# Kernel tuning notes

Measured on AMD Instinct MI355X. Metric: run time of the kernel, lower is better.

The kernel has to match this reference:

```python
import jax, jax.numpy as jnp
import numpy as np

D_MODEL = 1024
NUM_HEADS = 16
HEAD_DIM = D_MODEL // NUM_HEADS


def setup_inputs() -> dict:
    key = jax.random.key(0)
    ks = jax.random.split(key, 9)
    s = 1.0 / np.sqrt(D_MODEL)
    x = jax.random.normal(ks[0], (2, 2048, D_MODEL), dtype=jnp.float32)
    Wq = jax.random.uniform(ks[1], (D_MODEL, D_MODEL), jnp.float32, -s, s)
    bq = jax.random.uniform(ks[2], (D_MODEL,), jnp.float32, -s, s)
    Wk = jax.random.uniform(ks[3], (D_MODEL, D_MODEL), jnp.float32, -s, s)
    bk = jax.random.uniform(ks[4], (D_MODEL,), jnp.float32, -s, s)
    Wv = jax.random.uniform(ks[5], (D_MODEL, D_MODEL), jnp.float32, -s, s)
    bv = jax.random.uniform(ks[6], (D_MODEL,), jnp.float32, -s, s)
    Wo = jax.random.uniform(ks[7], (D_MODEL, D_MODEL), jnp.float32, -s, s)
    bo = jax.random.uniform(ks[8], (D_MODEL,), jnp.float32, -s, s)
    return {"x": x, "Wq": Wq, "bq": bq, "Wk": Wk, "bk": bk,
            "Wv": Wv, "bv": bv, "Wo": Wo, "bo": bo}


def reference(x, Wq, bq, Wk, bk, Wv, bv, Wo, bo):
    B, S, _ = x.shape
    def split_heads(t):  # [B,S,D] -> [B,H,S,hd]
        return t.reshape(B, S, NUM_HEADS, HEAD_DIM).transpose(0, 2, 1, 3)
    q = split_heads(x @ Wq + bq)
    k = split_heads(x @ Wk + bk)
    v = split_heads(x @ Wv + bv)
    scores = jnp.einsum('bhqd,bhkd->bhqk', q, k) / np.sqrt(HEAD_DIM)
    attn = jax.nn.softmax(scores, axis=-1)
    ctx = jnp.einsum('bhqk,bhkd->bhqd', attn, v)
    ctx = ctx.transpose(0, 2, 1, 3).reshape(B, S, D_MODEL)
    return ctx @ Wo + bo
```

## Files before the change

### kernel.cpp

```cpp
#include <hip/hip_runtime.h>
#include <stdint.h>

#define DM 1024
#define SEQ 2048
#define NTOK 4096
#define HD 64

typedef __bf16 bf16x8 __attribute__((ext_vector_type(8)));
typedef float f32x4 __attribute__((ext_vector_type(4)));
typedef uint32_t u32x2 __attribute__((ext_vector_type(2)));
typedef uint32_t u32x4 __attribute__((ext_vector_type(4)));

#if __has_builtin(__builtin_amdgcn_exp2f)
#define EXP2F(x) __builtin_amdgcn_exp2f(x)
#else
#define EXP2F(x) exp2f(x)
#endif

__device__ __forceinline__ void gll16f(const char* g, char* lds_wave_base, int lane) {
#if __has_builtin(__builtin_amdgcn_global_load_lds)
  __builtin_amdgcn_global_load_lds(
      (const __attribute__((address_space(1))) void*)g,
      (__attribute__((address_space(3))) void*)lds_wave_base, 16, 0, 0);
#else
  *(bf16x8*)(lds_wave_base + lane * 16) = *(const bf16x8*)g;
#endif
}

__device__ __forceinline__ uint16_t f2bf(float f) {
  uint32_t x = __float_as_uint(f);
  return (uint16_t)((x + 0x7fffu + ((x >> 16) & 1u)) >> 16);
}

__device__ __forceinline__ uint32_t cvtpk(float a, float b) {
  uint32_t r;
  asm("v_cvt_pk_bf16_f32 %0, %1, %2" : "=v"(r) : "v"(a), "v"(b));
  return r;
}

__device__ __forceinline__ bf16x8 mk8(uint32_t a, uint32_t b, uint32_t c, uint32_t d) {
  u32x4 t = {a, b, c, d};
  return __builtin_bit_cast(bf16x8, t);
}

__global__ void cvt_x_kernel(const float* __restrict__ x, uint16_t* __restrict__ xb) {
  int i = (blockIdx.x * 256 + threadIdx.x) * 4;
  float4 v = *(const float4*)&x[i];
  uint64_t pk = (uint64_t)f2bf(v.x) | ((uint64_t)f2bf(v.y) << 16) |
                ((uint64_t)f2bf(v.z) << 32) | ((uint64_t)f2bf(v.w) << 48);
  *(uint64_t*)&xb[i] = pk;
}

__global__ void twt4_kernel(const float* __restrict__ W0, const float* __restrict__ W1,
                            const float* __restrict__ W2, const float* __restrict__ W3,
                            uint16_t* __restrict__ T0, uint16_t* __restrict__ T1,
                            uint16_t* __restrict__ T2, uint16_t* __restrict__ T3) {
  __shared__ float t[32][33];
  int z = blockIdx.z;
  const float* W = (z == 0) ? W0 : (z == 1) ? W1 : (z == 2) ? W2 : W3;
  uint16_t* T = (z == 0) ? T0 : (z == 1) ? T1 : (z == 2) ? T2 : T3;
  int tx = threadIdx.x, ty = threadIdx.y;
  int kb = blockIdx.y * 32, nb = blockIdx.x * 32;
#pragma unroll
  for (int i = 0; i < 4; i++)
    t[ty + i * 8][tx] = W[(kb + ty + i * 8) * DM + nb + tx];
  __syncthreads();
#pragma unroll
  for (int i = 0; i < 4; i++)
    T[(nb + ty + i * 8) * DM + kb + tx] = f2bf(t[tx][ty + i * 8]);
}

template <int MODE, int MF>
__device__ __forceinline__ void gemm_body(const uint16_t* __restrict__ A,
                                          const uint16_t* __restrict__ Bt,
                                          const float* __restrict__ bias, float scale,
                                          void* __restrict__ out, uint16_t* lds) {
  const int tid = threadIdx.x;
  const int w = tid >> 6, lane = tid & 63;
  const int wr = w >> 1, wc = w & 1;
  const int a15 = lane & 15, a4 = lane >> 4;
  const int m0 = blockIdx.y * (MF * 32), n0 = blockIdx.x * 128;
  char* lgA = (char*)lds;
  char* lgB = (char*)(lds + MF * 2048);
  f32x4 acc[MF][4];
#pragma unroll
  for (int m = 0; m < MF; m++)
#pragma unroll
    for (int n = 0; n < 4; n++) acc[m][n] = (f32x4){0.f, 0.f, 0.f, 0.f};

  const char* Ag = (const char*)(A + (size_t)m0 * DM);
  const char* Bg = (const char*)(Bt + (size_t)n0 * DM);
  const int srow = lane >> 3;
  const int scol = ((lane & 7) * 16) ^ (srow << 4);
  const int swz = (a15 & 7) << 4;

  for (int k0 = 0; k0 < DM; k0 += 64) {
#pragma unroll
    for (int c = 0; c < MF; c++) {
      int ro = w * (MF * 8) + c * 8 + srow;
      gll16f(Ag + (size_t)ro * (DM * 2) + k0 * 2 + scol, lgA + (w * MF + c) * 1024, lane);
    }
#pragma unroll
    for (int c = 0; c < 4; c++) {
      int ro = w * 32 + c * 8 + srow;
      gll16f(Bg + (size_t)ro * (DM * 2) + k0 * 2 + scol, lgB + (w * 4 + c) * 1024, lane);
    }
    __syncthreads();
    bf16x8 af[MF][2], bfr[4][2];
#pragma unroll
    for (int m = 0; m < MF; m++)
#pragma unroll
      for (int kk = 0; kk < 2; kk++)
        af[m][kk] = *(const bf16x8*)(lgA + (wr * (MF * 16) + m * 16 + a15) * 128 +
                                     ((kk * 64 + a4 * 16) ^ swz));
#pragma unroll
    for (int n = 0; n < 4; n++)
#pragma unroll
      for (int kk = 0; kk < 2; kk++)
        bfr[n][kk] = *(const bf16x8*)(lgB + (wc * 64 + n * 16 + a15) * 128 +
                                      ((kk * 64 + a4 * 16) ^ swz));
#pragma unroll
    for (int kk = 0; kk < 2; kk++)
#pragma unroll
      for (int m = 0; m < MF; m++)
#pragma unroll
        for (int n = 0; n < 4; n++)
          acc[m][n] = __builtin_amdgcn_mfma_f32_16x16x32_bf16(af[m][kk], bfr[n][kk],
                                                              acc[m][n], 0, 0, 0);
    __syncthreads();
  }

#pragma unroll
  for (int m = 0; m < MF; m++) {
#pragma unroll
    for (int n = 0; n < 4; n++) {
      int gr0 = m0 + wr * (MF * 16) + m * 16 + a4 * 4;
      int col = n0 + wc * 64 + n * 16 + a15;
      float bv = bias[col];
      if constexpr (MODE == 2) {
        float* O = (float*)out;
#pragma unroll
        for (int j = 0; j < 4; j++)
          O[(size_t)(gr0 + j) * DM + col] = acc[m][n][j] + bv;
      } else if constexpr (MODE == 0) {
        uint16_t* O = (uint16_t*)out;
        int h = col >> 6, d = col & 63;
#pragma unroll
        for (int j = 0; j < 4; j++) {
          int gr = gr0 + j;
          int b = gr >> 11, s = gr & 2047;
          O[((size_t)(((b << 4) + h)) * SEQ + s) * HD + d] = f2bf((acc[m][n][j] + bv) * scale);
        }
      } else {
        uint16_t* O = (uint16_t*)out;
        int h = col >> 6, d = col & 63;
        int b = gr0 >> 11, s0 = gr0 & 2047;
        int it = s0 >> 6, s6 = s0 & 63;
        int pos = (s6 >> 5) * 32 + ((s6 >> 2) & 3) * 8 + ((s6 >> 4) & 1) * 4;
        uint64_t pk = 0;
#pragma unroll
        for (int j = 0; j < 4; j++)
          pk |= (uint64_t)f2bf(acc[m][n][j] + bv) << (16 * j);
        *(uint64_t*)&O[((size_t)(((b << 4) + h)) * HD + d) * SEQ + it * 64 + pos] = pk;
      }
    }
  }
}

#define CS_SCALE 0.180336880f

__global__ __launch_bounds__(256, 2) void gemm_qkv_kernel(
    const uint16_t* __restrict__ xb, const uint16_t* __restrict__ wtq,
    const uint16_t* __restrict__ wtk, const uint16_t* __restrict__ wtv,
    const float* __restrict__ bq, const float* __restrict__ bk,
    const float* __restrict__ bv, uint16_t* __restrict__ qo,
    uint16_t* __restrict__ ko, uint16_t* __restrict__ vto) {
  __shared__ __attribute__((aligned(16))) uint16_t lds[16384];
  int z = blockIdx.z;
  if (z == 0)      gemm_body<0, 4>(xb, wtq, bq, CS_SCALE, qo, lds);
  else if (z == 1) gemm_body<0, 4>(xb, wtk, bk, 1.0f, ko, lds);
  else             gemm_body<1, 4>(xb, wtv, bv, 1.0f, vto, lds);
}

__global__ __launch_bounds__(256, 2) void gemm_out_kernel(
    const uint16_t* __restrict__ ctx, const uint16_t* __restrict__ wto,
    const float* __restrict__ bo, float* __restrict__ out) {
  __shared__ __attribute__((aligned(16))) uint16_t lds[12288];
  gemm_body<2, 2>(ctx, wto, bo, 1.0f, out, lds);
}

__global__ __launch_bounds__(256, 2) void attn_kernel(
    const uint16_t* __restrict__ qg, const uint16_t* __restrict__ kg,
    const uint16_t* __restrict__ vtg, uint16_t* __restrict__ ctx) {
  const int tid = threadIdx.x;
  const int w = tid >> 6, l = tid & 63;
  const int l15 = l & 15, g = l >> 4;
  int id = blockIdx.x;
  int wg = (id & 7) * 64 + (id >> 3);
  int bh = wg >> 4, qb = wg & 15;
  const int q0 = qb * 128 + w * 32;
  const uint16_t* Qb = qg + (size_t)bh * SEQ * HD;
  const char* Kc = (const char*)(kg + (size_t)bh * SEQ * HD);
  const char* Vc = (const char*)(vtg + (size_t)bh * HD * SEQ);

  __shared__ __attribute__((aligned(16))) char Klds[2][8192];
  __shared__ __attribute__((aligned(16))) char Vlds[2][8192];

  const int srow = l >> 3;
  const int scolx = ((l & 7) * 16) ^ (srow << 4);

#define STAGE(BI, IT)                                                          \
  {                                                                            \
    const int it1_ = (IT);                                                     \
    _Pragma("unroll") for (int i = 0; i < 2; i++) {                            \
      int r = w * 16 + i * 8 + srow;                                           \
      gll16f(Kc + (size_t)(it1_ * 64 + r) * 128 + scolx,                       \
             &Klds[BI][w * 2048 + i * 1024], l);                               \
      gll16f(Vc + (size_t)r * (SEQ * 2) + it1_ * 128 + scolx,                  \
             &Vlds[BI][w * 2048 + i * 1024], l);                               \
    }                                                                          \
  }

  bf16x8 bq[2][2];
#pragma unroll
  for (int qs = 0; qs < 2; qs++)
#pragma unroll
    for (int ks = 0; ks < 2; ks++)
      bq[qs][ks] = *(const bf16x8*)&Qb[(size_t)(q0 + qs * 16 + l15) * HD + ks * 32 + g * 8];

  f32x4 o[4][2];
#pragma unroll
  for (int dt = 0; dt < 4; dt++)
#pragma unroll
    for (int qs = 0; qs < 2; qs++) o[dt][qs] = (f32x4){0.f, 0.f, 0.f, 0.f};
  f32x4 ol0 = {0.f, 0.f, 0.f, 0.f}, ol1 = {0.f, 0.f, 0.f, 0.f};
  const int swz = (l15 & 7) << 4;
  const uint32_t ONE2 = 0x3F803F80u;
  const bf16x8 aones = mk8(ONE2, ONE2, ONE2, ONE2);

  STAGE(0, 0);

#define ATTN_TILE(IT, BI, BN)                                                  \
  {                                                                            \
    const int it_ = (IT);                                                      \
    if (it_ + 1 < SEQ / 64) {                                                  \
      STAGE(BN, it_ + 1);                                                      \
      asm volatile("s_waitcnt vmcnt(4)\n\ts_barrier" ::: "memory");            \
    } else {                                                                   \
      asm volatile("s_waitcnt vmcnt(0)\n\ts_barrier" ::: "memory");            \
    }                                                                          \
                                            \
    bf16x8 ak[4][2];                                                           \
    _Pragma("unroll") for (int kt = 0; kt < 4; kt++)                           \
        _Pragma("unroll") for (int ks = 0; ks < 2; ks++)                       \
            ak[kt][ks] = *(const bf16x8*)&Klds[BI][(kt * 16 + l15) * 128 +     \
                                                   ((ks * 64 + g * 16) ^ swz)];\
                     \
    bf16x8 av[4][2];                                                           \
    _Pragma("unroll") for (int dt = 0; dt < 4; dt++)                           \
        _Pragma("unroll") for (int kb = 0; kb < 2; kb++)                       \
            av[dt][kb] = *(const bf16x8*)&Vlds[BI][(dt * 16 + l15) * 128 +     \
                                                   ((kb * 64 + g * 16) ^ swz)];\
                                           \
    f32x4 s[2][4];                                                             \
    _Pragma("unroll") for (int qs = 0; qs < 2; qs++)                           \
        _Pragma("unroll") for (int kt = 0; kt < 4; kt++)                       \
            s[qs][kt] = (f32x4){0.f, 0.f, 0.f, 0.f};                           \
    __builtin_amdgcn_s_setprio(1);                                             \
    _Pragma("unroll") for (int kt = 0; kt < 4; kt++)                           \
        _Pragma("unroll") for (int ks = 0; ks < 2; ks++) {                     \
      s[0][kt] = __builtin_amdgcn_mfma_f32_16x16x32_bf16(ak[kt][ks], bq[0][ks], s[0][kt], 0, 0, 0); \
      s[1][kt] = __builtin_amdgcn_mfma_f32_16x16x32_bf16(ak[kt][ks], bq[1][ks], s[1][kt], 0, 0, 0); \
    }                                                                          \
    __builtin_amdgcn_s_setprio(0);                                             \
        \
    float p0[4][4], p1[4][4];                                                  \
    _Pragma("unroll") for (int kt = 0; kt < 4; kt++)                           \
        _Pragma("unroll") for (int j = 0; j < 4; j++) {                        \
      p0[kt][j] = EXP2F(s[0][kt][j]);                                          \
      p1[kt][j] = EXP2F(s[1][kt][j]);                                          \
    }                                                                          \
    bf16x8 bp0[2], bp1[2];                                                     \
    _Pragma("unroll") for (int kb = 0; kb < 2; kb++) {                         \
      bp0[kb] = mk8(cvtpk(p0[2 * kb][0], p0[2 * kb][1]),                       \
                    cvtpk(p0[2 * kb][2], p0[2 * kb][3]),                       \
                    cvtpk(p0[2 * kb + 1][0], p0[2 * kb + 1][1]),               \
                    cvtpk(p0[2 * kb + 1][2], p0[2 * kb + 1][3]));              \
      bp1[kb] = mk8(cvtpk(p1[2 * kb][0], p1[2 * kb][1]),                       \
                    cvtpk(p1[2 * kb][2], p1[2 * kb][3]),                       \
                    cvtpk(p1[2 * kb + 1][0], p1[2 * kb + 1][1]),               \
                    cvtpk(p1[2 * kb + 1][2], p1[2 * kb + 1][3]));              \
    }                                                                          \
                                                \
    __builtin_amdgcn_s_setprio(1);                                             \
    _Pragma("unroll") for (int dt = 0; dt < 4; dt++)                           \
        _Pragma("unroll") for (int kb = 0; kb < 2; kb++) {                     \
      o[dt][0] = __builtin_amdgcn_mfma_f32_16x16x32_bf16(av[dt][kb], bp0[kb], o[dt][0], 0, 0, 0); \
      o[dt][1] = __builtin_amdgcn_mfma_f32_16x16x32_bf16(av[dt][kb], bp1[kb], o[dt][1], 0, 0, 0); \
    }                                                                          \
    _Pragma("unroll") for (int kb = 0; kb < 2; kb++) {                         \
      ol0 = __builtin_amdgcn_mfma_f32_16x16x32_bf16(aones, bp0[kb], ol0, 0, 0, 0); \
      ol1 = __builtin_amdgcn_mfma_f32_16x16x32_bf16(aones, bp1[kb], ol1, 0, 0, 0); \
    }                                                                          \
    __builtin_amdgcn_s_setprio(0);                                             \
    asm volatile("s_waitcnt lgkmcnt(0)\n\ts_barrier" ::: "memory");            \
  }

  for (int it2 = 0; it2 < SEQ / 128; ++it2) {
    ATTN_TILE(2 * it2, 0, 1);
    ATTN_TILE(2 * it2 + 1, 1, 0);
  }
#undef ATTN_TILE
#undef STAGE

  float inv0 = 1.0f / ol0[0];
  float inv1 = 1.0f / ol1[0];
  int b = bh >> 4, h = bh & 15;
  uint16_t* cr0 = ctx + (size_t)(b * SEQ + q0 + l15) * DM + h * HD + 4 * g;
  uint16_t* cr1 = cr0 + (size_t)16 * DM;
#pragma unroll
  for (int dt = 0; dt < 4; dt++) {
    u32x2 wv;
    wv[0] = cvtpk(o[dt][0][0] * inv0, o[dt][0][1] * inv0);
    wv[1] = cvtpk(o[dt][0][2] * inv0, o[dt][0][3] * inv0);
    *(u32x2*)&cr0[dt * 16] = wv;
    u32x2 wv2;
    wv2[0] = cvtpk(o[dt][1][0] * inv1, o[dt][1][1] * inv1);
    wv2[1] = cvtpk(o[dt][1][2] * inv1, o[dt][1][3] * inv1);
    *(u32x2*)&cr1[dt * 16] = wv2;
  }
}

extern "C" void kernel_launch(void* const* d_in, const int* in_sizes, int n_in,
                              void* d_out, int out_size, void* d_ws, size_t ws_size,
                              hipStream_t stream) {
  const float* x  = (const float*)d_in[0];
  const float* Wq = (const float*)d_in[1];
  const float* bq = (const float*)d_in[2];
  const float* Wk = (const float*)d_in[3];
  const float* bk = (const float*)d_in[4];
  const float* Wv = (const float*)d_in[5];
  const float* bv = (const float*)d_in[6];
  const float* Wo = (const float*)d_in[7];
  const float* bo = (const float*)d_in[8];

  char* ws = (char*)d_ws;
  uint16_t* xb  = (uint16_t*)(ws);
  uint16_t* wtq = (uint16_t*)(ws + 8388608);
  uint16_t* wtk = (uint16_t*)(ws + 10485760);
  uint16_t* wtv = (uint16_t*)(ws + 12582912);
  uint16_t* wto = (uint16_t*)(ws + 14680064);
  uint16_t* qb  = (uint16_t*)(ws + 16777216);
  uint16_t* kb  = (uint16_t*)(ws + 25165824);
  uint16_t* vtb = (uint16_t*)(ws + 33554432);
  uint16_t* ctx = xb;

  cvt_x_kernel<<<dim3(4096), dim3(256), 0, stream>>>(x, xb);
  twt4_kernel<<<dim3(32, 32, 4), dim3(32, 8), 0, stream>>>(
      Wq, Wk, Wv, Wo, wtq, wtk, wtv, wto);
  gemm_qkv_kernel<<<dim3(8, 32, 3), dim3(256), 0, stream>>>(
      xb, wtq, wtk, wtv, bq, bk, bv, qb, kb, vtb);
  attn_kernel<<<dim3(512), dim3(256), 0, stream>>>(qb, kb, vtb, ctx);
  gemm_out_kernel<<<dim3(8, 64), dim3(256), 0, stream>>>(ctx, wto, bo, (float*)d_out);
}
```

Measured before the change: 96.08 us.

## Merge prep kernels, swizzle GEMM block order, and deepen attention K/V prefetch

```diff
diff --git a/kernel.cpp b/kernel.cpp
--- a/kernel.cpp
+++ b/kernel.cpp
@@ -43,24 +43,27 @@
   return __builtin_bit_cast(bf16x8, t);
 }
 
-__global__ void cvt_x_kernel(const float* __restrict__ x, uint16_t* __restrict__ xb) {
-  int i = (blockIdx.x * 256 + threadIdx.x) * 4;
-  float4 v = *(const float4*)&x[i];
-  uint64_t pk = (uint64_t)f2bf(v.x) | ((uint64_t)f2bf(v.y) << 16) |
-                ((uint64_t)f2bf(v.z) << 32) | ((uint64_t)f2bf(v.w) << 48);
-  *(uint64_t*)&xb[i] = pk;
-}
-
-__global__ void twt4_kernel(const float* __restrict__ W0, const float* __restrict__ W1,
+__global__ void prep_kernel(const float* __restrict__ x, uint16_t* __restrict__ xb,
+                            const float* __restrict__ W0, const float* __restrict__ W1,
                             const float* __restrict__ W2, const float* __restrict__ W3,
                             uint16_t* __restrict__ T0, uint16_t* __restrict__ T1,
                             uint16_t* __restrict__ T2, uint16_t* __restrict__ T3) {
   __shared__ float t[32][33];
-  int z = blockIdx.z;
-  const float* W = (z == 0) ? W0 : (z == 1) ? W1 : (z == 2) ? W2 : W3;
-  uint16_t* T = (z == 0) ? T0 : (z == 1) ? T1 : (z == 2) ? T2 : T3;
-  int tx = threadIdx.x, ty = threadIdx.y;
-  int kb = blockIdx.y * 32, nb = blockIdx.x * 32;
+  int bid = blockIdx.x;
+  if (bid < 4096) {
+    int i = (bid * 256 + threadIdx.x) * 4;
+    float4 v = *(const float4*)&x[i];
+    uint64_t pk = (uint64_t)f2bf(v.x) | ((uint64_t)f2bf(v.y) << 16) |
+                  ((uint64_t)f2bf(v.z) << 32) | ((uint64_t)f2bf(v.w) << 48);
+    *(uint64_t*)&xb[i] = pk;
+    return;
+  }
+  int b2 = bid - 4096;
+  int zz = b2 >> 10, rr = b2 & 1023;
+  const float* W = (zz == 0) ? W0 : (zz == 1) ? W1 : (zz == 2) ? W2 : W3;
+  uint16_t* T = (zz == 0) ? T0 : (zz == 1) ? T1 : (zz == 2) ? T2 : T3;
+  int tx = threadIdx.x & 31, ty = threadIdx.x >> 5;
+  int nb = (rr & 31) * 32, kb = (rr >> 5) * 32;
 #pragma unroll
   for (int i = 0; i < 4; i++)
     t[ty + i * 8][tx] = W[(kb + ty + i * 8) * DM + nb + tx];
@@ -74,12 +77,13 @@
 __device__ __forceinline__ void gemm_body(const uint16_t* __restrict__ A,
                                           const uint16_t* __restrict__ Bt,
                                           const float* __restrict__ bias, float scale,
-                                          void* __restrict__ out, uint16_t* lds) {
+                                          void* __restrict__ out, uint16_t* lds,
+                                          int bx, int by) {
   const int tid = threadIdx.x;
   const int w = tid >> 6, lane = tid & 63;
   const int wr = w >> 1, wc = w & 1;
   const int a15 = lane & 15, a4 = lane >> 4;
-  const int m0 = blockIdx.y * (MF * 32), n0 = blockIdx.x * 128;
+  const int m0 = by * (MF * 32), n0 = bx * 128;
   char* lgA = (char*)lds;
   char* lgB = (char*)(lds + MF * 2048);
   f32x4 acc[MF][4];
@@ -176,17 +180,23 @@
     const float* __restrict__ bv, uint16_t* __restrict__ qo,
     uint16_t* __restrict__ ko, uint16_t* __restrict__ vto) {
   __shared__ __attribute__((aligned(16))) uint16_t lds[16384];
-  int z = blockIdx.z;
-  if (z == 0)      gemm_body<0, 4>(xb, wtq, bq, CS_SCALE, qo, lds);
-  else if (z == 1) gemm_body<0, 4>(xb, wtk, bk, 1.0f, ko, lds);
-  else             gemm_body<1, 4>(xb, wtv, bv, 1.0f, vto, lds);
+  int id = blockIdx.x;
+  int swz = (id & 7) * 96 + (id >> 3);
+  int z = swz >> 8, r = swz & 255;
+  int by = r >> 3, bx = r & 7;
+  if (z == 0)      gemm_body<0, 4>(xb, wtq, bq, CS_SCALE, qo, lds, bx, by);
+  else if (z == 1) gemm_body<0, 4>(xb, wtk, bk, 1.0f, ko, lds, bx, by);
+  else             gemm_body<1, 4>(xb, wtv, bv, 1.0f, vto, lds, bx, by);
 }
 
 __global__ __launch_bounds__(256, 2) void gemm_out_kernel(
     const uint16_t* __restrict__ ctx, const uint16_t* __restrict__ wto,
     const float* __restrict__ bo, float* __restrict__ out) {
   __shared__ __attribute__((aligned(16))) uint16_t lds[12288];
-  gemm_body<2, 2>(ctx, wto, bo, 1.0f, out, lds);
+  int id = blockIdx.x;
+  int swz = (id & 7) * 64 + (id >> 3);
+  int by = swz >> 3, bx = swz & 7;
+  gemm_body<2, 2>(ctx, wto, bo, 1.0f, out, lds, bx, by);
 }
 
 __global__ __launch_bounds__(256, 2) void attn_kernel(
@@ -203,8 +213,8 @@
   const char* Kc = (const char*)(kg + (size_t)bh * SEQ * HD);
   const char* Vc = (const char*)(vtg + (size_t)bh * HD * SEQ);
 
-  __shared__ __attribute__((aligned(16))) char Klds[2][8192];
-  __shared__ __attribute__((aligned(16))) char Vlds[2][8192];
+  __shared__ __attribute__((aligned(16))) char Klds[4][8192];
+  __shared__ __attribute__((aligned(16))) char Vlds[4][8192];
 
   const int srow = l >> 3;
   const int scolx = ((l & 7) * 16) ^ (srow << 4);
@@ -238,17 +248,8 @@
   const uint32_t ONE2 = 0x3F803F80u;
   const bf16x8 aones = mk8(ONE2, ONE2, ONE2, ONE2);
 
-  STAGE(0, 0);
-
-#define ATTN_TILE(IT, BI, BN)                                                  \
+#define TILE_BODY(BI)                                                          \
   {                                                                            \
-    const int it_ = (IT);                                                      \
-    if (it_ + 1 < SEQ / 64) {                                                  \
-      STAGE(BN, it_ + 1);                                                      \
-      asm volatile("s_waitcnt vmcnt(4)\n\ts_barrier" ::: "memory");            \
-    } else {                                                                   \
-      asm volatile("s_waitcnt vmcnt(0)\n\ts_barrier" ::: "memory");            \
-    }                                                                          \
                                             \
     bf16x8 ak[4][2];                                                           \
     _Pragma("unroll") for (int kt = 0; kt < 4; kt++)                           \
@@ -303,14 +304,31 @@
       ol1 = __builtin_amdgcn_mfma_f32_16x16x32_bf16(aones, bp1[kb], ol1, 0, 0, 0); \
     }                                                                          \
     __builtin_amdgcn_s_setprio(0);                                             \
-    asm volatile("s_waitcnt lgkmcnt(0)\n\ts_barrier" ::: "memory");            \
-  }
-
-  for (int it2 = 0; it2 < SEQ / 128; ++it2) {
-    ATTN_TILE(2 * it2, 0, 1);
-    ATTN_TILE(2 * it2 + 1, 1, 0);
-  }
-#undef ATTN_TILE
+  }
+
+  STAGE(0, 0);
+  STAGE(1, 1);
+
+  for (int it4 = 0; it4 < 8; ++it4) {
+    int tb = it4 * 4;
+    STAGE(2, tb + 2);
+    STAGE(3, tb + 3);
+    asm volatile("s_waitcnt vmcnt(8)\n\ts_barrier" ::: "memory");
+    TILE_BODY(0);
+    TILE_BODY(1);
+    asm volatile("s_waitcnt lgkmcnt(0)\n\ts_barrier" ::: "memory");
+    if (it4 < 7) {
+      STAGE(0, tb + 4);
+      STAGE(1, tb + 5);
+      asm volatile("s_waitcnt vmcnt(8)\n\ts_barrier" ::: "memory");
+    } else {
+      asm volatile("s_waitcnt vmcnt(0)\n\ts_barrier" ::: "memory");
+    }
+    TILE_BODY(2);
+    TILE_BODY(3);
+    asm volatile("s_waitcnt lgkmcnt(0)\n\ts_barrier" ::: "memory");
+  }
+#undef TILE_BODY
 #undef STAGE
 
   float inv0 = 1.0f / ol0[0];
@@ -355,11 +373,10 @@
   uint16_t* vtb = (uint16_t*)(ws + 33554432);
   uint16_t* ctx = xb;
 
-  cvt_x_kernel<<<dim3(4096), dim3(256), 0, stream>>>(x, xb);
-  twt4_kernel<<<dim3(32, 32, 4), dim3(32, 8), 0, stream>>>(
-      Wq, Wk, Wv, Wo, wtq, wtk, wtv, wto);
-  gemm_qkv_kernel<<<dim3(8, 32, 3), dim3(256), 0, stream>>>(
+  prep_kernel<<<dim3(8192), dim3(256), 0, stream>>>(
+      x, xb, Wq, Wk, Wv, Wo, wtq, wtk, wtv, wto);
+  gemm_qkv_kernel<<<dim3(768), dim3(256), 0, stream>>>(
       xb, wtq, wtk, wtv, bq, bk, bv, qb, kb, vtb);
   attn_kernel<<<dim3(512), dim3(256), 0, stream>>>(qb, kb, vtb, ctx);
-  gemm_out_kernel<<<dim3(8, 64), dim3(256), 0, stream>>>(ctx, wto, bo, (float*)d_out);
-}
+  gemm_out_kernel<<<dim3(512), dim3(256), 0, stream>>>(ctx, wto, bo, (float*)d_out);
+}
```

After: 92.18 us (median of 2 runs). 1.04x faster.
